# Kernel tuning notes

Hardware: AMD Instinct MI355X
Metric: run time of the kernel (lower is better)

## Reference

```python
import jax, jax.numpy as jnp
import numpy as np

B, N, H, T = 64, 64, 128, 128


def setup_inputs() -> dict:
    key = jax.random.key(0)
    ks = jax.random.split(key, 8)
    tf = jax.random.normal(ks[0], (B, N, H, T), dtype=jnp.float32)
    # learnable symmetric adjacency parameter
    ap = jax.random.normal(ks[1], (N, N), dtype=jnp.float32) * 0.1
    ap = (ap + ap.T) / 2
    # edge MLP params (stored as (in, out) for x @ W)
    W1 = jax.random.normal(ks[2], (2 * H, H), dtype=jnp.float32) * (1.0 / np.sqrt(2 * H))
    b1 = jnp.zeros((H,), dtype=jnp.float32)
    W2 = jax.random.normal(ks[3], (H, H // 2), dtype=jnp.float32) * (1.0 / np.sqrt(H))
    b2 = jnp.zeros((H // 2,), dtype=jnp.float32)
    W3 = jax.random.normal(ks[4], (H // 2, 1), dtype=jnp.float32) * (1.0 / np.sqrt(H // 2))
    b3 = jnp.zeros((1,), dtype=jnp.float32)
    return {"temporal_features": tf, "adj_param": ap, "W1": W1, "b1": b1,
            "W2": W2, "b2": b2, "W3": W3, "b3": b3}


def reference(temporal_features, adj_param, W1, b1, W2, b2, W3, b3):
    # node features: mean over time -> (B, N, H)
    node = temporal_features.mean(axis=-1)
    h_dim = node.shape[-1]
    # concat([h_i, h_j]) @ W1 == h_i @ W1[:H] + h_j @ W1[H:]  (avoids materializing 2H concat)
    Wi, Wj = W1[:h_dim], W1[h_dim:]
    pi = jnp.einsum('bnh,hk->bnk', node, Wi)  # (B, N, H)
    pj = jnp.einsum('bnh,hk->bnk', node, Wj)
    h = jax.nn.relu(pi[:, :, None, :] + pj[:, None, :, :] + b1)  # (B, N, N, H)
    # Dropout(0.2) is identity at inference
    h = jax.nn.relu(jnp.einsum('bijh,hk->bijk', h, W2) + b2)      # (B, N, N, H//2)
    feat_adj = (jnp.einsum('bijk,ko->bijo', h, W3) + b3)[..., 0]  # (B, N, N)
    # combined method
    adj = 0.5 * adj_param[None, :, :] + 0.5 * feat_adj
    # symmetrize + relu
    adj = jax.nn.relu((adj + jnp.swapaxes(adj, -2, -1)) / 2)
    # add self-loops and degree-normalize rows
    adj = adj + jnp.eye(adj.shape[-1], dtype=adj.dtype)[None]
    adj = adj / (adj.sum(axis=-1, keepdims=True) + 1e-8)
    return adj
```

## Files before the change

### kernel.cpp

```cpp
#include <hip/hip_runtime.h>
#include <stdint.h>
#include <stddef.h>

typedef __attribute__((ext_vector_type(8))) short short8;
typedef __attribute__((ext_vector_type(4))) float f32x4;
typedef __attribute__((ext_vector_type(4))) unsigned uint4v;

__device__ inline unsigned short f2bf(float x) {
    unsigned u = __float_as_uint(x);
    unsigned r = (u + 0x7fffu + ((u >> 16) & 1u)) >> 16;
    return (unsigned short)r;
}

__device__ inline unsigned pk2t(float lo, float hi) {
    return __builtin_amdgcn_perm(__float_as_uint(hi), __float_as_uint(lo), 0x07060302u);
}

template <int CTRL>
__device__ inline float dpp_add(float v) {
    int t = __builtin_amdgcn_update_dpp(0, __float_as_int(v), CTRL, 0xF, 0xF, true);
    return v + __int_as_float(t);
}
__device__ inline float row16_sum(float v) {
    v = dpp_add<0xB1>(v);
    v = dpp_add<0x4E>(v);
    v = dpp_add<0x124>(v);
    v = dpp_add<0x128>(v);
    return v;
}

__global__ __launch_bounds__(256) void k1_mean(const float* __restrict__ tf,
                                               float* __restrict__ node) {
    int wave = (blockIdx.x * blockDim.x + threadIdx.x) >> 6;
    int lane = threadIdx.x & 63;
    int half = lane >> 5;
    int c = lane & 31;
    const f32x4* tf4 = reinterpret_cast<const f32x4*>(tf);
    size_t base = (size_t)wave * 8 * 64;

    f32x4 v[8];
#pragma unroll
    for (int k = 0; k < 8; ++k) v[k] = __builtin_nontemporal_load(&tf4[base + (size_t)k * 64 + lane]);

    float s[8];
#pragma unroll
    for (int k = 0; k < 8; ++k) s[k] = (v[k][0] + v[k][1]) + (v[k][2] + v[k][3]);
#pragma unroll
    for (int m = 1; m <= 16; m <<= 1) {
#pragma unroll
        for (int k = 0; k < 8; ++k) s[k] += __shfl_xor(s[k], m);
    }
    if (c == 0) {
#pragma unroll
        for (int k = 0; k < 8; ++k) {
            int rp = wave * 8 + k;
            node[(size_t)rp * 2 + half] = s[k] * (1.0f / 128.0f);
        }
    }
}

__global__ __launch_bounds__(512) void k2_proj(const float* __restrict__ node,
                                               const float* __restrict__ W1,
                                               const float* __restrict__ b1,
                                               const float* __restrict__ W2,
                                               float* __restrict__ pi,
                                               float* __restrict__ pj,
                                               unsigned short* __restrict__ w2t_g) {
    const int LP = 136;
    __shared__ unsigned short A_lds[32 * LP];
    __shared__ unsigned short BT[128 * LP];
    __shared__ float b1s[128];

    int tid = threadIdx.x;
    int rblk = blockIdx.x >> 1;
    int half = blockIdx.x & 1;
    int r0 = rblk * 32;

    if (blockIdx.x < 16) {
        int idx = blockIdx.x * 512 + tid;
        int m = idx >> 7, k = idx & 127;
        w2t_g[idx] = f2bf(W2[(size_t)k * 64 + m]);
    }

    {
        int row = tid >> 4;
        int c0 = (tid & 15) * 8;
        const float4* src = reinterpret_cast<const float4*>(node + (size_t)(r0 + row) * 128 + c0);
        float4 va = src[0];
        float4 vb = src[1];
        short8 pk;
        pk[0] = (short)f2bf(va.x); pk[1] = (short)f2bf(va.y);
        pk[2] = (short)f2bf(va.z); pk[3] = (short)f2bf(va.w);
        pk[4] = (short)f2bf(vb.x); pk[5] = (short)f2bf(vb.y);
        pk[6] = (short)f2bf(vb.z); pk[7] = (short)f2bf(vb.w);
        *reinterpret_cast<short8*>(&A_lds[row * LP + c0]) = pk;
    }
    {
        int n = tid & 127;
        int kq = tid >> 7;
        const float* Wbase = W1 + (size_t)half * 128 * 128 + n;
#pragma unroll
        for (int g = 0; g < 4; ++g) {
            int kb = kq * 32 + g * 8;
            short8 pk;
#pragma unroll
            for (int e = 0; e < 8; ++e) pk[e] = (short)f2bf(Wbase[(size_t)(kb + e) * 128]);
            *reinterpret_cast<short8*>(&BT[n * LP + kb]) = pk;
        }
    }
    if (tid < 128) b1s[tid] = b1[tid];
    __syncthreads();

    int w = tid >> 6;
    int l = tid & 63;
    int lr = l & 15;
    int lg = l >> 4;
    int rt = w & 1;
    int cq = w >> 1;

    f32x4 acc[2] = {{0, 0, 0, 0}, {0, 0, 0, 0}};
#pragma unroll
    for (int ks = 0; ks < 4; ++ks) {
        int kb = ks * 32 + lg * 8;
        short8 afrag = *reinterpret_cast<const short8*>(&A_lds[(rt * 16 + lr) * LP + kb]);
#pragma unroll
        for (int nt = 0; nt < 2; ++nt) {
            short8 bfrag = *reinterpret_cast<const short8*>(&BT[(cq * 32 + nt * 16 + lr) * LP + kb]);
            acc[nt] = __builtin_amdgcn_mfma_f32_16x16x32_bf16(afrag, bfrag, acc[nt], 0, 0, 0);
        }
    }
    float* out = half ? pj : pi;
#pragma unroll
    for (int nt = 0; nt < 2; ++nt) {
        int col = cq * 32 + nt * 16 + lr;
        float bias = half ? 0.0f : b1s[col];
#pragma unroll
        for (int r = 0; r < 4; ++r) {
            int row = r0 + rt * 16 + lg * 4 + r;
            out[(size_t)row * 128 + col] = acc[nt][r] + bias;
        }
    }
}

__global__ __launch_bounds__(256) void k3_mlp(const float* __restrict__ pi,
                                              const float* __restrict__ pj,
                                              const unsigned short* __restrict__ w2t_g,
                                              const float* __restrict__ b2,
                                              const float* __restrict__ W3,
                                              const float* __restrict__ b3,
                                              float* __restrict__ F) {
    const int LDA = 136;
    __shared__ unsigned short W2T[64 * LDA];
    __shared__ float pipb8[8][128];
    __shared__ float b2s[64], w3s[64];

    int tid = threadIdx.x;
    int b = blockIdx.x >> 3;
    int it = blockIdx.x & 7;
    int i0 = it * 8;

    int w = tid >> 6;
    int l = tid & 63;
    int lr = l & 15;
    int lg = l >> 4;

    float pjreg[32];
    {
        const float* pjrow = pj + (size_t)(b * 64 + w * 16 + lr) * 128;
#pragma unroll
        for (int ks = 0; ks < 4; ++ks) {
            float4 q0 = *reinterpret_cast<const float4*>(pjrow + ks * 32 + lg * 8);
            float4 q1 = *reinterpret_cast<const float4*>(pjrow + ks * 32 + lg * 8 + 4);
            pjreg[ks * 8 + 0] = q0.x; pjreg[ks * 8 + 1] = q0.y;
            pjreg[ks * 8 + 2] = q0.z; pjreg[ks * 8 + 3] = q0.w;
            pjreg[ks * 8 + 4] = q1.x; pjreg[ks * 8 + 5] = q1.y;
            pjreg[ks * 8 + 6] = q1.z; pjreg[ks * 8 + 7] = q1.w;
        }
    }
    {
        int row = tid >> 5;
        int c4 = tid & 31;
        float4 v = reinterpret_cast<const float4*>(pi + ((size_t)(b * 64 + i0 + row) * 128))[c4];
        reinterpret_cast<float4*>(&pipb8[row][0])[c4] = v;
    }
    {
        int m = tid >> 2;
        int q = tid & 3;
        const uint4v* src = reinterpret_cast<const uint4v*>(w2t_g + (size_t)m * 128 + q * 32);
        uint4v* dst = reinterpret_cast<uint4v*>(&W2T[m * LDA + q * 32]);
#pragma unroll
        for (int e = 0; e < 4; ++e) dst[e] = src[e];
    }
    if (tid < 64) {
        b2s[tid] = b2[tid];
        w3s[tid] = W3[tid];
    }
    float b3v = b3[0];
    __syncthreads();

    short8 bfr[4][4];
#pragma unroll
    for (int ks = 0; ks < 4; ++ks) {
        int kb = ks * 32 + lg * 8;
#pragma unroll
        for (int nt = 0; nt < 4; ++nt)
            bfr[ks][nt] = *reinterpret_cast<const short8*>(&W2T[(nt * 16 + lr) * LDA + kb]);
    }

#pragma unroll 2
    for (int il = 0; il < 8; ++il) {
        f32x4 acc0 = {0.f, 0.f, 0.f, 0.f};
        f32x4 acc1 = {0.f, 0.f, 0.f, 0.f};
        f32x4 acc2 = {0.f, 0.f, 0.f, 0.f};
        f32x4 acc3 = {0.f, 0.f, 0.f, 0.f};
        const float4* prow = reinterpret_cast<const float4*>(&pipb8[il][0]);
#pragma unroll
        for (int ks = 0; ks < 4; ++ks) {
            float4 pa = prow[ks * 8 + lg * 2];
            float4 pb = prow[ks * 8 + lg * 2 + 1];
            unsigned au[4];
            au[0] = pk2t(fmaxf(pa.x + pjreg[ks * 8 + 0], 0.0f),
                         fmaxf(pa.y + pjreg[ks * 8 + 1], 0.0f));
            au[1] = pk2t(fmaxf(pa.z + pjreg[ks * 8 + 2], 0.0f),
                         fmaxf(pa.w + pjreg[ks * 8 + 3], 0.0f));
            au[2] = pk2t(fmaxf(pb.x + pjreg[ks * 8 + 4], 0.0f),
                         fmaxf(pb.y + pjreg[ks * 8 + 5], 0.0f));
            au[3] = pk2t(fmaxf(pb.z + pjreg[ks * 8 + 6], 0.0f),
                         fmaxf(pb.w + pjreg[ks * 8 + 7], 0.0f));
            short8 afrag = *reinterpret_cast<short8*>(au);
            acc0 = __builtin_amdgcn_mfma_f32_16x16x32_bf16(afrag, bfr[ks][0], acc0, 0, 0, 0);
            acc1 = __builtin_amdgcn_mfma_f32_16x16x32_bf16(afrag, bfr[ks][1], acc1, 0, 0, 0);
            acc2 = __builtin_amdgcn_mfma_f32_16x16x32_bf16(afrag, bfr[ks][2], acc2, 0, 0, 0);
            acc3 = __builtin_amdgcn_mfma_f32_16x16x32_bf16(afrag, bfr[ks][3], acc3, 0, 0, 0);
        }
        float part[4] = {0.f, 0.f, 0.f, 0.f};
#pragma unroll
        for (int mt = 0; mt < 4; ++mt) {
            int m = mt * 16 + lr;
            float w3 = w3s[m];
            float bb = b2s[m];
            f32x4 a = (mt == 0) ? acc0 : (mt == 1) ? acc1 : (mt == 2) ? acc2 : acc3;
#pragma unroll
            for (int r = 0; r < 4; ++r) {
                float h = fmaxf(a[r] + bb, 0.0f);
                part[r] += h * w3;
            }
        }
#pragma unroll
        for (int r = 0; r < 4; ++r) part[r] = row16_sum(part[r]);
        if (lr == 0) {
#pragma unroll
            for (int r = 0; r < 4; ++r) {
                int j = w * 16 + lg * 4 + r;
                F[((size_t)b * 64 + i0 + il) * 64 + j] = part[r] + b3v;
            }
        }
    }
}

__global__ __launch_bounds__(1024) void k4_final(const float* __restrict__ F,
                                                 const float* __restrict__ ap,
                                                 float* __restrict__ out) {
    __shared__ float s[64][65];
    int b = blockIdx.x;
    int tid = threadIdx.x;
    for (int idx = tid; idx < 4096; idx += 1024) {
        s[idx >> 6][idx & 63] = F[(size_t)b * 4096 + idx];
    }
    __syncthreads();
    int wv = tid >> 6, lane = tid & 63;
#pragma unroll
    for (int itr = 0; itr < 4; ++itr) {
        int i = wv * 4 + itr;
        float a_ij = ap[i * 64 + lane];
        float v = 0.5f * a_ij + 0.25f * (s[i][lane] + s[lane][i]);
        v = fmaxf(v, 0.0f);
        if (i == lane) v += 1.0f;
        float sum = v;
        sum += __shfl_xor(sum, 1);
        sum += __shfl_xor(sum, 2);
        sum += __shfl_xor(sum, 4);
        sum += __shfl_xor(sum, 8);
        sum += __shfl_xor(sum, 16);
        sum += __shfl_xor(sum, 32);
        out[(size_t)b * 4096 + i * 64 + lane] = v / (sum + 1e-8f);
    }
}

extern "C" void kernel_launch(void* const* d_in, const int* in_sizes, int n_in,
                              void* d_out, int out_size, void* d_ws, size_t ws_size,
                              hipStream_t stream) {
    const float* tf = (const float*)d_in[0];
    const float* ap = (const float*)d_in[1];
    const float* W1 = (const float*)d_in[2];
    const float* b1 = (const float*)d_in[3];
    const float* W2 = (const float*)d_in[4];
    const float* b2 = (const float*)d_in[5];
    const float* W3 = (const float*)d_in[6];
    const float* b3 = (const float*)d_in[7];
    float* out = (float*)d_out;

    char* ws = (char*)d_ws;
    float* node = (float*)(ws);
    float* pi   = (float*)(ws + (size_t)(2 << 20));
    float* pj   = (float*)(ws + (size_t)(4 << 20));
    float* F    = (float*)(ws + (size_t)(6 << 20));
    unsigned short* w2t_g = (unsigned short*)(ws + (size_t)(7 << 20));

    k1_mean<<<8192, 256, 0, stream>>>(tf, node);
    k2_proj<<<256, 512, 0, stream>>>(node, W1, b1, W2, pi, pj, w2t_g);
    k3_mlp<<<512, 256, 0, stream>>>(pi, pj, w2t_g, b2, W3, b3, F);
    k4_final<<<64, 1024, 0, stream>>>(F, ap, out);
}
```

Baseline: 66.60 us.

## Pre-convert W1 to bf16 transposed in mean kernel; split proj and final kernels finer

The mean kernel's first 64 blocks now convert W1 to a transposed bf16 copy in workspace. The projection kernel can then load B tiles with vector copies instead of doing strided fp32 loads and conversions in every block. The projection kernel also uses 16-row tiles across 512 blocks for more parallelism, though each block reloads the full weight tile. The final kernel is split into two 512-thread blocks per batch, which doubles the F staging loads in exchange for more blocks in flight.

After: 65.66 us, median of 2. Within noise of the previous version (-1.4%).

```diff
diff --git a/kernel.cpp b/kernel.cpp
--- a/kernel.cpp
+++ b/kernel.cpp
@@ -30,7 +30,19 @@
 }
 
 __global__ __launch_bounds__(256) void k1_mean(const float* __restrict__ tf,
-                                               float* __restrict__ node) {
+                                               const float* __restrict__ W1,
+                                               float* __restrict__ node,
+                                               unsigned short* __restrict__ w1t_g) {
+    if (blockIdx.x < 64) {
+        int base = blockIdx.x * 512 + threadIdx.x * 2;
+#pragma unroll
+        for (int e = 0; e < 2; ++e) {
+            int idx = base + e;
+            int c = idx >> 7, k = idx & 127;
+            int ch = c >> 7, n = c & 127;
+            w1t_g[idx] = f2bf(W1[(size_t)ch * 16384 + (size_t)k * 128 + n]);
+        }
+    }
     int wave = (blockIdx.x * blockDim.x + threadIdx.x) >> 6;
     int lane = threadIdx.x & 63;
     int half = lane >> 5;
@@ -60,21 +72,21 @@
 }
 
 __global__ __launch_bounds__(512) void k2_proj(const float* __restrict__ node,
-                                               const float* __restrict__ W1,
+                                               const unsigned short* __restrict__ w1t_g,
                                                const float* __restrict__ b1,
                                                const float* __restrict__ W2,
                                                float* __restrict__ pi,
                                                float* __restrict__ pj,
                                                unsigned short* __restrict__ w2t_g) {
     const int LP = 136;
-    __shared__ unsigned short A_lds[32 * LP];
+    __shared__ unsigned short A_lds[16 * LP];
     __shared__ unsigned short BT[128 * LP];
     __shared__ float b1s[128];
 
     int tid = threadIdx.x;
     int rblk = blockIdx.x >> 1;
     int half = blockIdx.x & 1;
-    int r0 = rblk * 32;
+    int r0 = rblk * 16;
 
     if (blockIdx.x < 16) {
         int idx = blockIdx.x * 512 + tid;
@@ -83,30 +95,21 @@
     }
 
     {
-        int row = tid >> 4;
-        int c0 = (tid & 15) * 8;
-        const float4* src = reinterpret_cast<const float4*>(node + (size_t)(r0 + row) * 128 + c0);
-        float4 va = src[0];
-        float4 vb = src[1];
-        short8 pk;
-        pk[0] = (short)f2bf(va.x); pk[1] = (short)f2bf(va.y);
-        pk[2] = (short)f2bf(va.z); pk[3] = (short)f2bf(va.w);
-        pk[4] = (short)f2bf(vb.x); pk[5] = (short)f2bf(vb.y);
-        pk[6] = (short)f2bf(vb.z); pk[7] = (short)f2bf(vb.w);
-        *reinterpret_cast<short8*>(&A_lds[row * LP + c0]) = pk;
-    }
-    {
-        int n = tid & 127;
-        int kq = tid >> 7;
-        const float* Wbase = W1 + (size_t)half * 128 * 128 + n;
-#pragma unroll
-        for (int g = 0; g < 4; ++g) {
-            int kb = kq * 32 + g * 8;
-            short8 pk;
-#pragma unroll
-            for (int e = 0; e < 8; ++e) pk[e] = (short)f2bf(Wbase[(size_t)(kb + e) * 128]);
-            *reinterpret_cast<short8*>(&BT[n * LP + kb]) = pk;
-        }
+        int row = tid >> 5;
+        int c0 = (tid & 31) * 4;
+        float4 v = *reinterpret_cast<const float4*>(node + (size_t)(r0 + row) * 128 + c0);
+        unsigned wb[2];
+        wb[0] = (unsigned)f2bf(v.x) | ((unsigned)f2bf(v.y) << 16);
+        wb[1] = (unsigned)f2bf(v.z) | ((unsigned)f2bf(v.w) << 16);
+        *reinterpret_cast<uint2*>(&A_lds[row * LP + c0]) = *reinterpret_cast<uint2*>(wb);
+    }
+    {
+        int n = tid >> 2;
+        int q = tid & 3;
+        const uint4v* src = reinterpret_cast<const uint4v*>(w1t_g + ((size_t)(half * 128 + n) * 128 + q * 32));
+        uint4v* dst = reinterpret_cast<uint4v*>(&BT[n * LP + q * 32]);
+#pragma unroll
+        for (int e = 0; e < 4; ++e) dst[e] = src[e];
     }
     if (tid < 128) b1s[tid] = b1[tid];
     __syncthreads();
@@ -115,30 +118,22 @@
     int l = tid & 63;
     int lr = l & 15;
     int lg = l >> 4;
-    int rt = w & 1;
-    int cq = w >> 1;
-
-    f32x4 acc[2] = {{0, 0, 0, 0}, {0, 0, 0, 0}};
+
+    f32x4 acc = {0, 0, 0, 0};
 #pragma unroll
     for (int ks = 0; ks < 4; ++ks) {
         int kb = ks * 32 + lg * 8;
-        short8 afrag = *reinterpret_cast<const short8*>(&A_lds[(rt * 16 + lr) * LP + kb]);
-#pragma unroll
-        for (int nt = 0; nt < 2; ++nt) {
-            short8 bfrag = *reinterpret_cast<const short8*>(&BT[(cq * 32 + nt * 16 + lr) * LP + kb]);
-            acc[nt] = __builtin_amdgcn_mfma_f32_16x16x32_bf16(afrag, bfrag, acc[nt], 0, 0, 0);
-        }
+        short8 afrag = *reinterpret_cast<const short8*>(&A_lds[lr * LP + kb]);
+        short8 bfrag = *reinterpret_cast<const short8*>(&BT[(w * 16 + lr) * LP + kb]);
+        acc = __builtin_amdgcn_mfma_f32_16x16x32_bf16(afrag, bfrag, acc, 0, 0, 0);
     }
     float* out = half ? pj : pi;
-#pragma unroll
-    for (int nt = 0; nt < 2; ++nt) {
-        int col = cq * 32 + nt * 16 + lr;
-        float bias = half ? 0.0f : b1s[col];
-#pragma unroll
-        for (int r = 0; r < 4; ++r) {
-            int row = r0 + rt * 16 + lg * 4 + r;
-            out[(size_t)row * 128 + col] = acc[nt][r] + bias;
-        }
+    int col = w * 16 + lr;
+    float bias = half ? 0.0f : b1s[col];
+#pragma unroll
+    for (int r = 0; r < 4; ++r) {
+        int row = r0 + lg * 4 + r;
+        out[(size_t)row * 128 + col] = acc[r] + bias;
     }
 }
 
@@ -258,20 +253,21 @@
     }
 }
 
-__global__ __launch_bounds__(1024) void k4_final(const float* __restrict__ F,
-                                                 const float* __restrict__ ap,
-                                                 float* __restrict__ out) {
+__global__ __launch_bounds__(512) void k4_final(const float* __restrict__ F,
+                                                const float* __restrict__ ap,
+                                                float* __restrict__ out) {
     __shared__ float s[64][65];
-    int b = blockIdx.x;
+    int b = blockIdx.x >> 1;
+    int rh = (blockIdx.x & 1) * 32;
     int tid = threadIdx.x;
-    for (int idx = tid; idx < 4096; idx += 1024) {
+    for (int idx = tid; idx < 4096; idx += 512) {
         s[idx >> 6][idx & 63] = F[(size_t)b * 4096 + idx];
     }
     __syncthreads();
     int wv = tid >> 6, lane = tid & 63;
 #pragma unroll
     for (int itr = 0; itr < 4; ++itr) {
-        int i = wv * 4 + itr;
+        int i = rh + wv * 4 + itr;
         float a_ij = ap[i * 64 + lane];
         float v = 0.5f * a_ij + 0.25f * (s[i][lane] + s[lane][i]);
         v = fmaxf(v, 0.0f);
@@ -306,9 +302,10 @@
     float* pj   = (float*)(ws + (size_t)(4 << 20));
     float* F    = (float*)(ws + (size_t)(6 << 20));
     unsigned short* w2t_g = (unsigned short*)(ws + (size_t)(7 << 20));
-
-    k1_mean<<<8192, 256, 0, stream>>>(tf, node);
-    k2_proj<<<256, 512, 0, stream>>>(node, W1, b1, W2, pi, pj, w2t_g);
+    unsigned short* w1t_g = (unsigned short*)(ws + (size_t)(7 << 20) + 65536);
+
+    k1_mean<<<8192, 256, 0, stream>>>(tf, W1, node, w1t_g);
+    k2_proj<<<512, 512, 0, stream>>>(node, w1t_g, b1, W2, pi, pj, w2t_g);
     k3_mlp<<<512, 256, 0, stream>>>(pi, pj, w2t_g, b2, W3, b3, F);
-    k4_final<<<64, 1024, 0, stream>>>(F, ap, out);
-}
+    k4_final<<<128, 512, 0, stream>>>(F, ap, out);
+}
```
